# Optimization experiments

Measured on AMD Instinct MI355X. Metric: run time of the kernel, lower is better.

The kernel has to match this reference:

```python
import jax, jax.numpy as jnp
import numpy as np

N_NODES = 50000
N_EDGES = 1600000
D = 128
L = 4
N_GRAPHS = 512


def setup_inputs() -> dict:
    key = jax.random.key(0)
    ks = jax.random.split(key, 8)
    x = jax.random.normal(ks[0], (N_NODES, D), dtype=jnp.float32)
    edge_index = jax.random.randint(ks[1], (2, N_EDGES), 0, N_NODES, dtype=jnp.int64)
    batch = jnp.sort(jax.random.randint(ks[2], (N_NODES,), 0, N_GRAPHS, dtype=jnp.int64))
    # MLP params per GIN layer: Linear(D->D), ReLU, Linear(D->D). Stacked over L layers.
    s = 1.0 / np.sqrt(D)
    Ws1 = jax.random.uniform(ks[3], (L, D, D), jnp.float32, -s, s)
    bs1 = jax.random.uniform(ks[4], (L, D), jnp.float32, -s, s)
    Ws2 = jax.random.uniform(ks[5], (L, D, D), jnp.float32, -s, s)
    bs2 = jax.random.uniform(ks[6], (L, D), jnp.float32, -s, s)
    return {"x": x, "edge_index": edge_index, "batch": batch,
            "Ws1": Ws1, "bs1": bs1, "Ws2": Ws2, "bs2": bs2}


def reference(x, edge_index, batch, Ws1, bs1, Ws2, bs2):
    src, dst = edge_index[0], edge_index[1]
    for l in range(L):
        # GINConv (eps=0): h = MLP(x + sum_{j in N(i)} x_j)
        agg = jax.ops.segment_sum(x[src], dst, num_segments=N_NODES)  # [N, D]
        h = x + agg
        h = jax.nn.relu(h @ Ws1[l] + bs1[l])
        x = h @ Ws2[l] + bs2[l]
    # global_add_pool: segment-sum node features by graph id
    return jax.ops.segment_sum(x, batch, num_segments=N_GRAPHS)  # [G, D]
```

## Files before the change

### kernel.cpp

```cpp
#include <hip/hip_runtime.h>

#define NN 50000
#define NE 1600000
#define DD 128
#define NL 4
#define NG 512
#define BSH 7
#define BMSK 127
#define NBUK 391
#define NBLK 196
#define EPB 8192
#define HN (NBUK * NBLK)
#define HT 150
#define EPT 20
#define CVT_N (NN * DD / 4)
#define PREP_N (NL * DD * DD)

typedef __attribute__((ext_vector_type(8))) short short8;
typedef __attribute__((ext_vector_type(4))) float floatx4;

__device__ __forceinline__ unsigned short f2bf(float f) {
    unsigned int u = __float_as_uint(f);
    u += 0x7fffu + ((u >> 16) & 1u);
    return (unsigned short)(u >> 16);
}
__device__ __forceinline__ float bf2f(unsigned short u) {
    return __uint_as_float(((unsigned int)u) << 16);
}

__global__ __launch_bounds__(512) void prelude_kernel(
    const float* __restrict__ x0, const float* __restrict__ Ws1,
    const float* __restrict__ Ws2, const int* __restrict__ src,
    unsigned short* __restrict__ xbf, unsigned short* __restrict__ W1T,
    unsigned short* __restrict__ W2T, int* __restrict__ hist) {
    __shared__ int h[NBUK];
    int tid = threadIdx.x, bid = blockIdx.x;
    int gid = bid * 512 + tid;
    for (int idx = gid; idx < CVT_N; idx += NBLK * 512) {
        float4 f = ((const float4*)x0)[idx];
        ushort4 o;
        o.x = f2bf(f.x); o.y = f2bf(f.y); o.z = f2bf(f.z); o.w = f2bf(f.w);
        ((ushort4*)xbf)[idx] = o;
    }
    for (int idx = gid; idx < PREP_N; idx += NBLK * 512) {
        int l = idx >> 14, rem = idx & 16383;
        int k = rem >> 7, n = rem & 127;
        int o = (l << 14) + (n << 7) + k;
        W1T[o] = f2bf(Ws1[idx]);
        W2T[o] = f2bf(Ws2[idx]);
    }
    for (int i = tid; i < NBUK; i += 512) h[i] = 0;
    __syncthreads();
    {
        int base = bid * EPB;
        int end = base + EPB; if (end > NE) end = NE;
        for (int e = base + tid; e < end; e += 512) atomicAdd(&h[src[e] >> BSH], 1);
    }
    __syncthreads();
    for (int i = tid; i < NBUK; i += 512) hist[i * NBLK + bid] = h[i];
}

__global__ __launch_bounds__(512) void scan_lb_kernel(const int* __restrict__ in,
                                                      int* __restrict__ out,
                                                      unsigned int* __restrict__ tstat,
                                                      int n) {
    __shared__ int s[512];
    int b = blockIdx.x, tid = threadIdx.x;
    int i = b * 512 + tid;
    int v = (i < n) ? in[i] : 0;
    s[tid] = v;
    __syncthreads();
    for (int off = 1; off < 512; off <<= 1) {
        int u = (tid >= off) ? s[tid - off] : 0;
        __syncthreads();
        s[tid] += u;
        __syncthreads();
    }
    int incl = s[tid];
    int agg = s[511];
    if (tid == 0)
        __hip_atomic_store(&tstat[b], 0x80000000u | (unsigned int)agg,
                           __ATOMIC_RELAXED, __HIP_MEMORY_SCOPE_AGENT);
    unsigned int got = 0;
    if (tid < b) {
        unsigned int x = __hip_atomic_load(&tstat[tid], __ATOMIC_RELAXED,
                                           __HIP_MEMORY_SCOPE_AGENT);
        while (!(x & 0x80000000u)) {
            __builtin_amdgcn_s_sleep(1);
            x = __hip_atomic_load(&tstat[tid], __ATOMIC_RELAXED,
                                  __HIP_MEMORY_SCOPE_AGENT);
        }
        got = x & 0x7FFFFFFFu;
    }
    __syncthreads();
    s[tid] = (int)got;
    __syncthreads();
    for (int off = 256; off > 0; off >>= 1) {
        if (tid < off) s[tid] += s[tid + off];
        __syncthreads();
    }
    int carry = s[0];
    if (i < n) out[i] = carry + incl - v;
}


__global__ __launch_bounds__(512) void sscatter_kernel(const int* __restrict__ src,
                                                       const int* __restrict__ dst,
                                                       const int* __restrict__ soff,
                                                       unsigned int* __restrict__ ebufA) {
    __shared__ int h[NBUK];
    int tid = threadIdx.x;
    for (int i = tid; i < NBUK; i += 512) h[i] = 0;
    __syncthreads();
    int base = blockIdx.x * EPB;
#pragma unroll
    for (int it = 0; it < EPB / 512; it++) {
        int e = base + it * 512 + tid;
        if (e < NE) {
            int s = src[e];
            int ss = s >> BSH;
            int p = atomicAdd(&h[ss], 1);
            ebufA[soff[ss * NBLK + blockIdx.x] + p] =
                ((unsigned int)dst[e] << 16) | (unsigned int)s;
        }
    }
}

__global__ __launch_bounds__(512) void bhist_kernel(const unsigned int* __restrict__ ebufA,
                                                    int* __restrict__ hist) {
    __shared__ int h[NBUK];
    int tid = threadIdx.x;
    for (int i = tid; i < NBUK; i += 512) h[i] = 0;
    __syncthreads();
    int base = blockIdx.x * EPB;
#pragma unroll
    for (int it = 0; it < EPB / 512; it++) {
        int e = base + it * 512 + tid;
        if (e < NE) atomicAdd(&h[ebufA[e] >> (16 + BSH)], 1);
    }
    __syncthreads();
    for (int i = tid; i < NBUK; i += 512) hist[i * NBLK + blockIdx.x] = h[i];
}

__global__ __launch_bounds__(512) void bscatter_kernel(const unsigned int* __restrict__ ebufA,
                                                       const int* __restrict__ bkoff,
                                                       int* __restrict__ ebuf) {
    __shared__ int h[NBUK];
    int tid = threadIdx.x;
    for (int i = tid; i < NBUK; i += 512) h[i] = 0;
    __syncthreads();
    int base = blockIdx.x * EPB;
#pragma unroll
    for (int it = 0; it < EPB / 512; it++) {
        int e = base + it * 512 + tid;
        if (e < NE) {
            unsigned int pk = ebufA[e];
            int d = pk >> 16;
            int s = pk & 0xFFFF;
            int bu = d >> BSH;
            int p = atomicAdd(&h[bu], 1);
            ebuf[bkoff[bu * NBLK + blockIdx.x] + p] = (s << BSH) | (d & BMSK);
        }
    }
}

__global__ __launch_bounds__(256) void bucket_csr_kernel(const int* __restrict__ ebuf,
                                                         const int* __restrict__ bkoff,
                                                         int* __restrict__ rowptr,
                                                         int* __restrict__ rowend,
                                                         int* __restrict__ col) {
    __shared__ int cnt[128], exc[128], ebase[128];
    int b = blockIdx.x, tid = threadIdx.x;
    int segstart = bkoff[b * NBLK];
    int segend = (b < NBUK - 1) ? bkoff[(b + 1) * NBLK] : NE;
    if (tid < 128) cnt[tid] = 0;
    __syncthreads();
    int evr[EPT];
    int rnk[EPT];
#pragma unroll
    for (int j = 0; j < EPT; j++) {
        int i = segstart + tid + j * 256;
        if (i < segend) {
            int ev = ebuf[i];
            evr[j] = ev;
            rnk[j] = atomicAdd(&cnt[ev & BMSK], 1);
        } else {
            evr[j] = -1;
        }
    }
    __syncthreads();
    int v = (tid < 128) ? cnt[tid] : 0;
    if (tid < 128) exc[tid] = v;
    __syncthreads();
    for (int off = 1; off < 128; off <<= 1) {
        int u = (tid < 128 && tid >= off) ? exc[tid - off] : 0;
        __syncthreads();
        if (tid < 128) exc[tid] += u;
        __syncthreads();
    }
    if (tid < 128) {
        int excl = exc[tid] - v;
        ebase[tid] = segstart + excl;
        int node = (b << BSH) + tid;
        if (node < NN) {
            rowptr[node] = segstart + excl;
            rowend[node] = segstart + excl + v;
        }
    }
    __syncthreads();
#pragma unroll
    for (int j = 0; j < EPT; j++) {
        if (evr[j] >= 0) {
            int low = evr[j] & BMSK;
            col[ebase[low] + rnk[j]] = ((unsigned)evr[j]) >> BSH;
        }
    }
}

__global__ __launch_bounds__(256) void agg_kernel(const unsigned short* __restrict__ xbf,
                                                  const int* __restrict__ rowptr,
                                                  const int* __restrict__ rowend,
                                                  const int* __restrict__ col,
                                                  unsigned short* __restrict__ hpre) {
    int g = threadIdx.x >> 4;
    int lane = threadIdx.x & 15;
    int node = blockIdx.x * 16 + g;
    const uint4* base = (const uint4*)xbf;
    float a[8];
    {
        uint4 v = base[node * 16 + lane];
        a[0] = __uint_as_float(v.x << 16); a[1] = __uint_as_float(v.x & 0xFFFF0000u);
        a[2] = __uint_as_float(v.y << 16); a[3] = __uint_as_float(v.y & 0xFFFF0000u);
        a[4] = __uint_as_float(v.z << 16); a[5] = __uint_as_float(v.z & 0xFFFF0000u);
        a[6] = __uint_as_float(v.w << 16); a[7] = __uint_as_float(v.w & 0xFFFF0000u);
    }
    int s = rowptr[node], e = rowend[node];
    int i = s;
    for (; i + 8 <= e; i += 8) {
        uint4 v0 = base[col[i] * 16 + lane];
        uint4 v1 = base[col[i + 1] * 16 + lane];
        uint4 v2 = base[col[i + 2] * 16 + lane];
        uint4 v3 = base[col[i + 3] * 16 + lane];
        uint4 v4 = base[col[i + 4] * 16 + lane];
        uint4 v5 = base[col[i + 5] * 16 + lane];
        uint4 v6 = base[col[i + 6] * 16 + lane];
        uint4 v7 = base[col[i + 7] * 16 + lane];
#define ACC(V)                                                            \
        a[0] += __uint_as_float(V.x << 16); a[1] += __uint_as_float(V.x & 0xFFFF0000u); \
        a[2] += __uint_as_float(V.y << 16); a[3] += __uint_as_float(V.y & 0xFFFF0000u); \
        a[4] += __uint_as_float(V.z << 16); a[5] += __uint_as_float(V.z & 0xFFFF0000u); \
        a[6] += __uint_as_float(V.w << 16); a[7] += __uint_as_float(V.w & 0xFFFF0000u)
        ACC(v0); ACC(v1); ACC(v2); ACC(v3); ACC(v4); ACC(v5); ACC(v6); ACC(v7);
    }
    for (; i < e; i++) {
        uint4 v = base[col[i] * 16 + lane];
        ACC(v);
    }
#undef ACC
    uint4 o;
    o.x = (unsigned int)f2bf(a[0]) | ((unsigned int)f2bf(a[1]) << 16);
    o.y = (unsigned int)f2bf(a[2]) | ((unsigned int)f2bf(a[3]) << 16);
    o.z = (unsigned int)f2bf(a[4]) | ((unsigned int)f2bf(a[5]) << 16);
    o.w = (unsigned int)f2bf(a[6]) | ((unsigned int)f2bf(a[7]) << 16);
    ((uint4*)hpre)[node * 16 + lane] = o;
}

__global__ __launch_bounds__(256) void mlp_kernel(const unsigned short* __restrict__ A,
                                                  const unsigned short* __restrict__ W1,
                                                  const float* __restrict__ b1,
                                                  const unsigned short* __restrict__ W2,
                                                  const float* __restrict__ b2,
                                                  unsigned short* __restrict__ O) {
    __shared__ unsigned short Wl[128 * 128];
    __shared__ unsigned short Hl[128 * 128];
    int tid = threadIdx.x;
    int wg = tid >> 6;
    int lane = tid & 63;
    int quad = lane >> 4;
    int li = lane & 15;
    int mg = wg >> 1, ng = wg & 1;
    int rowb = blockIdx.x * 128;

    {
        const uint4* wgl = (const uint4*)W1;
#pragma unroll
        for (int it = 0; it < 8; it++) {
            int idx = it * 256 + tid;
            int n = idx >> 4, kc = idx & 15;
            *(uint4*)&Wl[n * 128 + ((kc * 8) ^ ((n & 7) << 3))] = wgl[idx];
        }
    }
    __syncthreads();

    floatx4 acc[4][4];
#pragma unroll
    for (int tn = 0; tn < 4; tn++)
#pragma unroll
        for (int mi = 0; mi < 4; mi++) acc[tn][mi] = (floatx4){0.f, 0.f, 0.f, 0.f};

#pragma unroll
    for (int kk = 0; kk < 4; kk++) {
        int kc = kk * 32 + quad * 8;
        short8 xf[4];
#pragma unroll
        for (int mi = 0; mi < 4; mi++) {
            int ar = rowb + mg * 64 + mi * 16 + li;
            xf[mi] = (ar < NN) ? *(const short8*)(A + (size_t)ar * DD + kc)
                               : (short8){0, 0, 0, 0, 0, 0, 0, 0};
        }
#pragma unroll
        for (int tn = 0; tn < 4; tn++) {
            int wr = ng * 64 + tn * 16 + li;
            short8 wf = *(const short8*)&Wl[wr * 128 + (kc ^ ((wr & 7) << 3))];
#pragma unroll
            for (int mi = 0; mi < 4; mi++)
                acc[tn][mi] = __builtin_amdgcn_mfma_f32_16x16x32_bf16(wf, xf[mi], acc[tn][mi], 0, 0, 0);
        }
    }

#pragma unroll
    for (int tn = 0; tn < 4; tn++) {
        float4 bv = ((const float4*)b1)[ng * 16 + tn * 4 + quad];
#pragma unroll
        for (int mi = 0; mi < 4; mi++) {
            int hr = mg * 64 + mi * 16 + li;
            float v0 = fmaxf(acc[tn][mi][0] + bv.x, 0.f);
            float v1 = fmaxf(acc[tn][mi][1] + bv.y, 0.f);
            float v2 = fmaxf(acc[tn][mi][2] + bv.z, 0.f);
            float v3 = fmaxf(acc[tn][mi][3] + bv.w, 0.f);
            uint2 u;
            u.x = (unsigned int)f2bf(v0) | ((unsigned int)f2bf(v1) << 16);
            u.y = (unsigned int)f2bf(v2) | ((unsigned int)f2bf(v3) << 16);
            int c = (ng * 64 + tn * 16 + quad * 4) ^ ((hr & 7) << 3);
            *(uint2*)&Hl[hr * 128 + c] = u;
        }
    }
    __syncthreads();

    {
        const uint4* wgl = (const uint4*)W2;
#pragma unroll
        for (int it = 0; it < 8; it++) {
            int idx = it * 256 + tid;
            int n = idx >> 4, kc = idx & 15;
            *(uint4*)&Wl[n * 128 + ((kc * 8) ^ ((n & 7) << 3))] = wgl[idx];
        }
    }
    __syncthreads();

#pragma unroll
    for (int tn = 0; tn < 4; tn++)
#pragma unroll
        for (int mi = 0; mi < 4; mi++) acc[tn][mi] = (floatx4){0.f, 0.f, 0.f, 0.f};

#pragma unroll
    for (int kk = 0; kk < 4; kk++) {
        int kc = kk * 32 + quad * 8;
        short8 hf[4];
#pragma unroll
        for (int mi = 0; mi < 4; mi++) {
            int hr = mg * 64 + mi * 16 + li;
            hf[mi] = *(const short8*)&Hl[hr * 128 + (kc ^ ((hr & 7) << 3))];
        }
#pragma unroll
        for (int tn = 0; tn < 4; tn++) {
            int wr = ng * 64 + tn * 16 + li;
            short8 wf = *(const short8*)&Wl[wr * 128 + (kc ^ ((wr & 7) << 3))];
#pragma unroll
            for (int mi = 0; mi < 4; mi++)
                acc[tn][mi] = __builtin_amdgcn_mfma_f32_16x16x32_bf16(wf, hf[mi], acc[tn][mi], 0, 0, 0);
        }
    }

#pragma unroll
    for (int tn = 0; tn < 4; tn++) {
        float4 bv = ((const float4*)b2)[ng * 16 + tn * 4 + quad];
#pragma unroll
        for (int mi = 0; mi < 4; mi++) {
            int m = rowb + mg * 64 + mi * 16 + li;
            if (m < NN) {
                uint2 u;
                u.x = (unsigned int)f2bf(acc[tn][mi][0] + bv.x) |
                      ((unsigned int)f2bf(acc[tn][mi][1] + bv.y) << 16);
                u.y = (unsigned int)f2bf(acc[tn][mi][2] + bv.z) |
                      ((unsigned int)f2bf(acc[tn][mi][3] + bv.w) << 16);
                *(uint2*)&O[(size_t)m * DD + ng * 64 + tn * 16 + quad * 4] = u;
            }
        }
    }
}

__global__ __launch_bounds__(128) void pool_kernel(const unsigned short* __restrict__ x,
                                                   const int* __restrict__ batch,
                                                   float* __restrict__ out) {
    int g = blockIdx.x;
    int lo = 0, hi = NN;
    while (lo < hi) { int mid = (lo + hi) >> 1; if (batch[mid] < g) lo = mid + 1; else hi = mid; }
    int s = lo;
    hi = NN;
    while (lo < hi) { int mid = (lo + hi) >> 1; if (batch[mid] < g + 1) lo = mid + 1; else hi = mid; }
    int e = lo;
    int d = threadIdx.x;
    float acc = 0.f;
    for (int i = s; i < e; i++) acc += bf2f(x[(size_t)i * DD + d]);
    out[g * DD + d] = acc;
}

extern "C" void kernel_launch(void* const* d_in, const int* in_sizes, int n_in,
                              void* d_out, int out_size, void* d_ws, size_t ws_size,
                              hipStream_t stream) {
    const float* x0 = (const float*)d_in[0];
    const int* edge = (const int*)d_in[1];
    const int* batch = (const int*)d_in[2];
    const float* Ws1 = (const float*)d_in[3];
    const float* bs1 = (const float*)d_in[4];
    const float* Ws2 = (const float*)d_in[5];
    const float* bs2 = (const float*)d_in[6];
    float* out = (float*)d_out;
    const int* src = edge;
    const int* dst = edge + NE;

    char* ws = (char*)d_ws;
    size_t off = 0;
    auto alloc = [&](size_t bytes) {
        void* p = ws + off;
        off += (bytes + 255) & ~(size_t)255;
        return p;
    };
    unsigned short* x0bf = (unsigned short*)alloc((size_t)NN * DD * 2);
    unsigned short* xA = (unsigned short*)alloc((size_t)NN * DD * 2);
    unsigned short* xB = (unsigned short*)alloc((size_t)NN * DD * 2);
    unsigned short* hpre = (unsigned short*)alloc((size_t)NN * DD * 2);
    int* col = (int*)alloc((size_t)NE * 4);
    int* ebuf = (int*)alloc((size_t)NE * 4);
    unsigned int* ebufA = (unsigned int*)alloc((size_t)NE * 4);
    int* hist = (int*)alloc((size_t)HN * 4);
    int* bkoff = (int*)alloc((size_t)HN * 4);
    int* soff = (int*)alloc((size_t)HN * 4);
    int* rowptr = (int*)alloc((size_t)(NN + 1) * 4);
    int* rowend = (int*)alloc((size_t)NN * 4);
    unsigned short* W1T = (unsigned short*)alloc((size_t)NL * DD * DD * 2);
    unsigned short* W2T = (unsigned short*)alloc((size_t)NL * DD * DD * 2);
    unsigned int* tstat = (unsigned int*)alloc(4096);
    unsigned int* tstatA = tstat;
    unsigned int* tstatB = tstat + 512;

    (void)hipMemsetAsync(tstat, 0, 4096, stream);
    prelude_kernel<<<NBLK, 512, 0, stream>>>(x0, Ws1, Ws2, src, x0bf, W1T, W2T, hist);
    scan_lb_kernel<<<HT, 512, 0, stream>>>(hist, soff, tstatA, HN);
    sscatter_kernel<<<NBLK, 512, 0, stream>>>(src, dst, soff, ebufA);
    bhist_kernel<<<NBLK, 512, 0, stream>>>(ebufA, hist);
    scan_lb_kernel<<<HT, 512, 0, stream>>>(hist, bkoff, tstatB, HN);
    bscatter_kernel<<<NBLK, 512, 0, stream>>>(ebufA, bkoff, ebuf);
    bucket_csr_kernel<<<NBUK, 256, 0, stream>>>(ebuf, bkoff, rowptr, rowend, col);

    const unsigned short* xin = x0bf;
    unsigned short* bufs[2] = {xA, xB};
    const int mlp_grid = (NN + 127) / 128;
    for (int l = 0; l < NL; l++) {
        agg_kernel<<<NN / 16, 256, 0, stream>>>(xin, rowptr, rowend, col, hpre);
        unsigned short* xout = bufs[l & 1];
        mlp_kernel<<<mlp_grid, 256, 0, stream>>>(hpre, W1T + l * DD * DD, bs1 + l * DD,
                                                 W2T + l * DD * DD, bs2 + l * DD, xout);
        xin = xout;
    }
    pool_kernel<<<NG, 128, 0, stream>>>(xin, batch, out);
}
```

Measured before the change: 449.4 us.

## Drop source-bucket pre-sort pass and bucket edges directly by destination

The CSR build previously did a two-pass radix-style sort: first scattering edges by source bucket, then histogramming and scattering again by destination bucket. This removes the source pass (sscatter, bhist and one scan), so the prelude histograms destination buckets and bscatter reads src/dst directly. It cuts three kernel launches and a full pass over the edge buffer. The risk is that the final column order within each row is no longer sorted by source, which may make the gathers in aggregation less local.

```diff
diff --git a/kernel.cpp b/kernel.cpp
--- a/kernel.cpp
+++ b/kernel.cpp
@@ -30,7 +30,7 @@
 
 __global__ __launch_bounds__(512) void prelude_kernel(
     const float* __restrict__ x0, const float* __restrict__ Ws1,
-    const float* __restrict__ Ws2, const int* __restrict__ src,
+    const float* __restrict__ Ws2, const int* __restrict__ dst,
     unsigned short* __restrict__ xbf, unsigned short* __restrict__ W1T,
     unsigned short* __restrict__ W2T, int* __restrict__ hist) {
     __shared__ int h[NBUK];
@@ -54,7 +54,7 @@
     {
         int base = bid * EPB;
         int end = base + EPB; if (end > NE) end = NE;
-        for (int e = base + tid; e < end; e += 512) atomicAdd(&h[src[e] >> BSH], 1);
+        for (int e = base + tid; e < end; e += 512) atomicAdd(&h[dst[e] >> BSH], 1);
     }
     __syncthreads();
     for (int i = tid; i < NBUK; i += 512) hist[i * NBLK + bid] = h[i];
@@ -103,46 +103,8 @@
     if (i < n) out[i] = carry + incl - v;
 }
 
-
-__global__ __launch_bounds__(512) void sscatter_kernel(const int* __restrict__ src,
+__global__ __launch_bounds__(512) void bscatter_kernel(const int* __restrict__ src,
                                                        const int* __restrict__ dst,
-                                                       const int* __restrict__ soff,
-                                                       unsigned int* __restrict__ ebufA) {
-    __shared__ int h[NBUK];
-    int tid = threadIdx.x;
-    for (int i = tid; i < NBUK; i += 512) h[i] = 0;
-    __syncthreads();
-    int base = blockIdx.x * EPB;
-#pragma unroll
-    for (int it = 0; it < EPB / 512; it++) {
-        int e = base + it * 512 + tid;
-        if (e < NE) {
-            int s = src[e];
-            int ss = s >> BSH;
-            int p = atomicAdd(&h[ss], 1);
-            ebufA[soff[ss * NBLK + blockIdx.x] + p] =
-                ((unsigned int)dst[e] << 16) | (unsigned int)s;
-        }
-    }
-}
-
-__global__ __launch_bounds__(512) void bhist_kernel(const unsigned int* __restrict__ ebufA,
-                                                    int* __restrict__ hist) {
-    __shared__ int h[NBUK];
-    int tid = threadIdx.x;
-    for (int i = tid; i < NBUK; i += 512) h[i] = 0;
-    __syncthreads();
-    int base = blockIdx.x * EPB;
-#pragma unroll
-    for (int it = 0; it < EPB / 512; it++) {
-        int e = base + it * 512 + tid;
-        if (e < NE) atomicAdd(&h[ebufA[e] >> (16 + BSH)], 1);
-    }
-    __syncthreads();
-    for (int i = tid; i < NBUK; i += 512) hist[i * NBLK + blockIdx.x] = h[i];
-}
-
-__global__ __launch_bounds__(512) void bscatter_kernel(const unsigned int* __restrict__ ebufA,
                                                        const int* __restrict__ bkoff,
                                                        int* __restrict__ ebuf) {
     __shared__ int h[NBUK];
@@ -154,12 +116,10 @@
     for (int it = 0; it < EPB / 512; it++) {
         int e = base + it * 512 + tid;
         if (e < NE) {
-            unsigned int pk = ebufA[e];
-            int d = pk >> 16;
-            int s = pk & 0xFFFF;
+            int d = dst[e];
             int bu = d >> BSH;
             int p = atomicAdd(&h[bu], 1);
-            ebuf[bkoff[bu * NBLK + blockIdx.x] + p] = (s << BSH) | (d & BMSK);
+            ebuf[bkoff[bu * NBLK + blockIdx.x] + p] = (src[e] << BSH) | (d & BMSK);
         }
     }
 }
@@ -433,25 +393,18 @@
     unsigned short* hpre = (unsigned short*)alloc((size_t)NN * DD * 2);
     int* col = (int*)alloc((size_t)NE * 4);
     int* ebuf = (int*)alloc((size_t)NE * 4);
-    unsigned int* ebufA = (unsigned int*)alloc((size_t)NE * 4);
     int* hist = (int*)alloc((size_t)HN * 4);
     int* bkoff = (int*)alloc((size_t)HN * 4);
-    int* soff = (int*)alloc((size_t)HN * 4);
     int* rowptr = (int*)alloc((size_t)(NN + 1) * 4);
     int* rowend = (int*)alloc((size_t)NN * 4);
     unsigned short* W1T = (unsigned short*)alloc((size_t)NL * DD * DD * 2);
     unsigned short* W2T = (unsigned short*)alloc((size_t)NL * DD * DD * 2);
-    unsigned int* tstat = (unsigned int*)alloc(4096);
-    unsigned int* tstatA = tstat;
-    unsigned int* tstatB = tstat + 512;
-
-    (void)hipMemsetAsync(tstat, 0, 4096, stream);
-    prelude_kernel<<<NBLK, 512, 0, stream>>>(x0, Ws1, Ws2, src, x0bf, W1T, W2T, hist);
-    scan_lb_kernel<<<HT, 512, 0, stream>>>(hist, soff, tstatA, HN);
-    sscatter_kernel<<<NBLK, 512, 0, stream>>>(src, dst, soff, ebufA);
-    bhist_kernel<<<NBLK, 512, 0, stream>>>(ebufA, hist);
-    scan_lb_kernel<<<HT, 512, 0, stream>>>(hist, bkoff, tstatB, HN);
-    bscatter_kernel<<<NBLK, 512, 0, stream>>>(ebufA, bkoff, ebuf);
+    unsigned int* tstat = (unsigned int*)alloc(2048);
+
+    (void)hipMemsetAsync(tstat, 0, 2048, stream);
+    prelude_kernel<<<NBLK, 512, 0, stream>>>(x0, Ws1, Ws2, dst, x0bf, W1T, W2T, hist);
+    scan_lb_kernel<<<HT, 512, 0, stream>>>(hist, bkoff, tstat, HN);
+    bscatter_kernel<<<NBLK, 512, 0, stream>>>(src, dst, bkoff, ebuf);
     bucket_csr_kernel<<<NBUK, 256, 0, stream>>>(ebuf, bkoff, rowptr, rowend, col);
 
     const unsigned short* xin = x0bf;
```

Result: faster. 434.8 us (-3.2%).
